# Kernel tuning notes

Hardware: AMD Instinct MI355X
Metric: run time of the kernel (lower is better)

## Reference

```python
import jax, jax.numpy as jnp
import numpy as np

N_NODES = 50000


def _gcn_norm(edge_index, num_nodes):
    # PyG GCNConv default: add self-loops, symmetric deg^{-1/2} normalization.
    src, dst = edge_index[0], edge_index[1]
    loops = jnp.arange(num_nodes, dtype=src.dtype)
    src = jnp.concatenate([src, loops])
    dst = jnp.concatenate([dst, loops])
    ones = jnp.ones(src.shape[0], dtype=jnp.float32)
    deg = jax.ops.segment_sum(ones, dst, num_segments=num_nodes)
    dinv = jnp.where(deg > 0, jax.lax.rsqrt(deg), 0.0)
    norm = dinv[src] * dinv[dst]  # [E + N]
    return src, dst, norm


def _gcn_layer(x, src, dst, norm, W, b, num_nodes):
    h = x @ W                                   # [N, H]
    msg = h[src] * norm[:, None]                # gather + scale, [E+N, H]
    out = jax.ops.segment_sum(msg, dst, num_segments=num_nodes)  # scatter-add
    return out + b


def setup_inputs() -> dict:
    key = jax.random.key(0)
    ks = jax.random.split(key, 8)
    d_in, d_h = 128, 128
    x = jax.random.normal(ks[0], (N_NODES, d_in), dtype=jnp.float32)
    edge_index = jax.random.randint(ks[1], (2, 800000), 0, N_NODES, dtype=jnp.int64)
    s1 = 1.0 / np.sqrt(d_in)
    s2 = 1.0 / np.sqrt(d_h)
    W1 = jax.random.normal(ks[2], (d_in, d_h), dtype=jnp.float32) * s1
    b1 = jnp.zeros((d_h,), dtype=jnp.float32)
    W2 = jax.random.normal(ks[3], (d_h, d_h), dtype=jnp.float32) * s2
    b2 = jnp.zeros((d_h,), dtype=jnp.float32)
    Wl = jax.random.normal(ks[4], (d_h, 1), dtype=jnp.float32) * s2
    bl = jnp.zeros((1,), dtype=jnp.float32)
    return {"x": x, "edge_index": edge_index, "W1": W1, "b1": b1,
            "W2": W2, "b2": b2, "Wl": Wl, "bl": bl}


def reference(x, edge_index, W1, b1, W2, b2, Wl, bl):
    n = x.shape[0]
    src, dst, norm = _gcn_norm(edge_index, n)
    h = jax.nn.relu(_gcn_layer(x, src, dst, norm, W1, b1, n))
    # dropout is identity in eval mode
    h = _gcn_layer(h, src, dst, norm, W2, b2, n)
    return jax.nn.sigmoid(h @ Wl + bl)  # [N, 1]
```

## Files before the change

kernel.cpp:

```cpp
#include <hip/hip_runtime.h>
#include <math.h>

#define NN 50000
#define NE 800000
#define DD 128
#define NPAD 50048
#define ELLW 64

typedef __attribute__((ext_vector_type(8))) short bf16x8;
typedef __attribute__((ext_vector_type(4))) float f32x4;
typedef __attribute__((ext_vector_type(2))) float f32x2;

__device__ __forceinline__ int clampN(int v) {
  return v < 0 ? 0 : (v >= NN ? NN - 1 : v);
}

__device__ __forceinline__ unsigned short f2b(float f) {
  union { float f; unsigned int u; } x; x.f = f;
  unsigned int u = x.u;
  u += 0x7fffu + ((u >> 16) & 1u);
  return (unsigned short)(u >> 16);
}

__device__ __forceinline__ float blo(unsigned int v) {
  union { unsigned int u; float f; } a; a.u = v << 16; return a.f;
}
__device__ __forceinline__ float bhi(unsigned int v) {
  union { unsigned int u; float f; } a; a.u = v & 0xffff0000u; return a.f;
}


__global__ __launch_bounds__(256) void k_prep_w(
    const float* __restrict__ W1, const float* __restrict__ W2,
    const float* __restrict__ b2, const float* __restrict__ Wl,
    const float* __restrict__ bl, unsigned short* __restrict__ Wt1,
    float* __restrict__ w2l, float* __restrict__ c0b, int* __restrict__ cur) {
  __shared__ float part[2];
  if (blockIdx.x < 64) {
    int i = blockIdx.x * 256 + threadIdx.x;
    int n = i >> 7, k = i & 127;
    Wt1[i] = f2b(W1[k * DD + n]);
  } else if (blockIdx.x == 64) {
    if (threadIdx.x < DD) {
      int k = threadIdx.x;
      float acc = 0.f;
      for (int c = 0; c < DD; ++c) acc += W2[k * DD + c] * Wl[c];
      w2l[k] = acc;
      float pc = b2[k] * Wl[k];
#pragma unroll
      for (int off = 32; off > 0; off >>= 1) pc += __shfl_down(pc, off, 64);
      if ((k & 63) == 0) part[k >> 6] = pc;
      __syncthreads();
      if (k == 0) c0b[0] = part[0] + part[1] + bl[0];
    }
  } else {
    int i = (blockIdx.x - 65) * 256 + threadIdx.x;
    if (i < NN) cur[i] = 0;
  }
}


__device__ __forceinline__ void scat1(int d, int s, int* __restrict__ cur,
                                      unsigned short* __restrict__ col) {
  d = clampN(d);
  int pos = atomicAdd(&cur[d], 1);
  if (pos < ELLW)
    __builtin_nontemporal_store((unsigned short)clampN(s), &col[d * ELLW + pos]);
}

__global__ __launch_bounds__(256) void k_scatter_nt(
    const int4* __restrict__ src4, const int4* __restrict__ dst4,
    int* __restrict__ cur, unsigned short* __restrict__ col) {
  int i = blockIdx.x * 256 + threadIdx.x;
  if (i < NE / 4) {
    int4 d4 = dst4[i];
    int4 s4 = src4[i];
    scat1(d4.x, s4.x, cur, col);
    scat1(d4.y, s4.y, cur, col);
    scat1(d4.z, s4.z, cur, col);
    scat1(d4.w, s4.w, cur, col);
  }
}


__global__ __launch_bounds__(256) void k_gemm_f32(
    const float* __restrict__ x, const unsigned short* __restrict__ Wt,
    const int* __restrict__ cur, unsigned short* __restrict__ outb) {
  __shared__ char lds[16384 + 32768];
  char* Al = lds;
  char* Wl = lds + 16384;

  const int tid = threadIdx.x;
  const int row0 = blockIdx.x * 64;

  {
    const float4* src = (const float4*)x;
#pragma unroll
    for (int kk = 0; kk < 8; ++kk) {
      int idx = tid + kk * 256;
      int r = idx >> 5;
      int c4 = idx & 31;
      float4 v = make_float4(0.f, 0.f, 0.f, 0.f);
      if (row0 + r < NN) v = src[(size_t)(row0 + r) * 32 + c4];
      ushort4 u;
      u.x = f2b(v.x); u.y = f2b(v.y); u.z = f2b(v.z); u.w = f2b(v.w);
      int bo = r * 256 + c4 * 8;
      *(ushort4*)(Al + (bo ^ ((r & 7) << 4))) = u;
    }
  }
  {
    const uint4* src = (const uint4*)Wt;
    for (int idx = tid; idx < 2048; idx += 256) {
      int bo = idx * 16;
      int r = bo >> 8;
      *(uint4*)(Wl + (bo ^ ((r & 7) << 4))) = src[idx];
    }
  }
  __syncthreads();

  const int w = tid >> 6, lane = tid & 63;
  const int lr = lane & 15, lk = lane >> 4;

  bf16x8 af[4];
  {
    int ar = w * 16 + lr;
    int base = ar * 256 + lk * 16;
    int swz = (ar & 7) << 4;
#pragma unroll
    for (int k4 = 0; k4 < 4; ++k4)
      af[k4] = *(const bf16x8*)(Al + ((base + k4 * 64) ^ swz));
  }

  f32x4 accs[8];
#pragma unroll
  for (int n = 0; n < 8; ++n) {
    f32x4 acc = {0.f, 0.f, 0.f, 0.f};
    int br = n * 16 + lr;
    int bbase = br * 256 + lk * 16;
    int bswz = (br & 7) << 4;
#pragma unroll
    for (int k4 = 0; k4 < 4; ++k4) {
      bf16x8 bf = *(const bf16x8*)(Wl + ((bbase + k4 * 64) ^ bswz));
      acc = __builtin_amdgcn_mfma_f32_16x16x32_bf16(af[k4], bf, acc, 0, 0, 0);
    }
    accs[n] = acc;
  }

#pragma unroll
  for (int r = 0; r < 4; ++r) {
    int grow = row0 + w * 16 + lk * 4 + r;
    if (grow < NN) {
      float dv = rsqrtf(1.0f + (float)cur[grow]);
#pragma unroll
      for (int n = 0; n < 8; ++n)
        outb[(size_t)grow * DD + n * 16 + lr] = f2b(accs[n][r] * dv);
    }
  }
}


__device__ __forceinline__ void accp(f32x2* acc, uint4 v) {
  f32x2 a0 = {blo(v.x), bhi(v.x)};
  f32x2 a1 = {blo(v.y), bhi(v.y)};
  f32x2 a2 = {blo(v.z), bhi(v.z)};
  f32x2 a3 = {blo(v.w), bhi(v.w)};
  acc[0] += a0;
  acc[1] += a1;
  acc[2] += a2;
  acc[3] += a3;
}

__global__ __launch_bounds__(256) void k_agg_relu_proj_ell(
    const uint4* __restrict__ tpb4, const float* __restrict__ b,
    const float* __restrict__ w2l, const int* __restrict__ cur,
    const unsigned short* __restrict__ col, float* __restrict__ s_out) {
  int wid = threadIdx.x >> 6;
  int lane = threadIdx.x & 63;
  int d = blockIdx.x * 4 + wid;
  int il = lane & 7, g = lane >> 3;

  f32x2 acc[8];
#pragma unroll
  for (int j = 0; j < 8; ++j) acc[j] = (f32x2){0.f, 0.f};

  int degd = cur[d];
  int deg = min(degd, ELLW);
  const unsigned short* crow = col + d * ELLW;
  for (int e = g; e < deg; e += 8) {
    int s = crow[e];
    uint4 v0 = tpb4[(size_t)s * 16 + il * 2];
    uint4 v1 = tpb4[(size_t)s * 16 + il * 2 + 1];
    accp(acc, v0);
    accp(acc + 4, v1);
  }
#pragma unroll
  for (int j = 0; j < 8; ++j) {
    float ax = acc[j].x, ay = acc[j].y;
    ax += __shfl_xor(ax, 8, 64);  ay += __shfl_xor(ay, 8, 64);
    ax += __shfl_xor(ax, 16, 64); ay += __shfl_xor(ay, 16, 64);
    ax += __shfl_xor(ax, 32, 64); ay += __shfl_xor(ay, 32, 64);
    acc[j].x = ax; acc[j].y = ay;
  }
  uint4 s0 = tpb4[(size_t)d * 16 + il * 2];
  uint4 s1 = tpb4[(size_t)d * 16 + il * 2 + 1];
  accp(acc, s0);
  accp(acc + 4, s1);

  float dv = rsqrtf(1.0f + (float)degd);
  float p = 0.f;
#pragma unroll
  for (int q = 0; q < 4; ++q) {
    float4 bb = ((const float4*)b)[il * 4 + q];
    float4 ww = ((const float4*)w2l)[il * 4 + q];
    p = fmaf(fmaxf(fmaf(dv, acc[2 * q].x, bb.x), 0.f), ww.x, p);
    p = fmaf(fmaxf(fmaf(dv, acc[2 * q].y, bb.y), 0.f), ww.y, p);
    p = fmaf(fmaxf(fmaf(dv, acc[2 * q + 1].x, bb.z), 0.f), ww.z, p);
    p = fmaf(fmaxf(fmaf(dv, acc[2 * q + 1].y, bb.w), 0.f), ww.w, p);
  }
  p += __shfl_xor(p, 1, 64);
  p += __shfl_xor(p, 2, 64);
  p += __shfl_xor(p, 4, 64);
  if (lane == 0) s_out[d] = dv * p;
}


__global__ __launch_bounds__(256) void k_agg_scalar_ell(
    const float* __restrict__ s, const float* __restrict__ c0b,
    const int* __restrict__ cur, const unsigned short* __restrict__ col,
    float* __restrict__ out) {
  int wid = threadIdx.x >> 6;
  int lane = threadIdx.x & 63;
  int q = lane & 15;
  int d = blockIdx.x * 16 + wid * 4 + (lane >> 4);

  int degd = cur[d];
  int deg = min(degd, ELLW);
  const unsigned short* crow = col + d * ELLW;
  float tot = 0.f;
  for (int e = q; e < deg; e += 16) tot += s[crow[e]];
  tot += __shfl_xor(tot, 1, 64);
  tot += __shfl_xor(tot, 2, 64);
  tot += __shfl_xor(tot, 4, 64);
  tot += __shfl_xor(tot, 8, 64);
  if (q == 0) {
    float dv = rsqrtf(1.0f + (float)degd);
    float z = dv * (tot + s[d]) + c0b[0];
    out[d] = 1.f / (1.f + expf(-z));
  }
}


extern "C" void kernel_launch(void* const* d_in, const int* in_sizes, int n_in,
                              void* d_out, int out_size, void* d_ws, size_t ws_size,
                              hipStream_t stream) {
  const float* x = (const float*)d_in[0];
  const int* ei = (const int*)d_in[1];
  const float* W1 = (const float*)d_in[2];
  const float* b1 = (const float*)d_in[3];
  const float* W2 = (const float*)d_in[4];
  const float* b2 = (const float*)d_in[5];
  const float* Wl = (const float*)d_in[6];
  const float* bl = (const float*)d_in[7];
  float* out = (float*)d_out;

  char* ws = (char*)d_ws;
  size_t off = 0;
  auto alloc = [&](size_t bytes) -> char* {
    char* p = ws + off;
    off = (off + bytes + 255) & ~(size_t)255;
    return p;
  };
  int* cur = (int*)alloc(NN * sizeof(int));
  unsigned short* colell = (unsigned short*)alloc((size_t)NN * ELLW * 2);
  unsigned short* Wt1 = (unsigned short*)alloc(DD * DD * 2);
  float* w2l = (float*)alloc(DD * sizeof(float));
  float* c0b = (float*)alloc(sizeof(float));
  unsigned short* tpb = (unsigned short*)alloc((size_t)NPAD * DD * 2);
  float* sbuf = (float*)alloc(NN * sizeof(float));
  (void)ws_size;

  k_prep_w<<<65 + 196, 256, 0, stream>>>(W1, W2, b2, Wl, bl, Wt1, w2l, c0b, cur);

  k_scatter_nt<<<(NE / 4 + 255) / 256, 256, 0, stream>>>(
      (const int4*)ei, (const int4*)(ei + NE), cur, colell);

  k_gemm_f32<<<NPAD / 64, 256, 0, stream>>>(x, Wt1, cur, tpb);

  k_agg_relu_proj_ell<<<NN / 4, 256, 0, stream>>>((const uint4*)tpb, b1, w2l,
                                                  cur, colell, sbuf);
  k_agg_scalar_ell<<<(NN + 15) / 16, 256, 0, stream>>>(sbuf, c0b, cur, colell, out);
}
```

Before: 127.7 us.

## Partition edge scatter into eight destination slices for XCD locality

The ELL-building scatter now runs eight times as many blocks. Each group of blocks handles only destinations inside one of eight node-range slices, with the slice chosen from the low bits of the block index, so consecutive blocks cover different slices. The intent is to keep the atomic counters and column writes of each slice local to one XCD's L2 on the multi-die GPU and to cut cross-die atomic traffic. The nontemporal stores become regular stores. The cost is that every dst vector is read eight times, and src is read only when some lane falls in the slice.

```diff
diff --git a/kernel.cpp b/kernel.cpp
--- a/kernel.cpp
+++ b/kernel.cpp
@@ -5,6 +5,7 @@
 #define NE 800000
 #define DD 128
 #define NPAD 50048
+#define NSLICE 6256
 #define ELLW 64
 
 typedef __attribute__((ext_vector_type(8))) short bf16x8;
@@ -60,25 +61,35 @@
 }
 
 
-__device__ __forceinline__ void scat1(int d, int s, int* __restrict__ cur,
+__device__ __forceinline__ void scat1(int d, int s, int lo, int hi,
+                                      int* __restrict__ cur,
                                       unsigned short* __restrict__ col) {
-  d = clampN(d);
-  int pos = atomicAdd(&cur[d], 1);
-  if (pos < ELLW)
-    __builtin_nontemporal_store((unsigned short)clampN(s), &col[d * ELLW + pos]);
-}
-
-__global__ __launch_bounds__(256) void k_scatter_nt(
+  if (d >= lo && d < hi) {
+    int pos = atomicAdd(&cur[d], 1);
+    if (pos < ELLW) col[d * ELLW + pos] = (unsigned short)clampN(s);
+  }
+}
+
+__global__ __launch_bounds__(256) void k_scatter4(
     const int4* __restrict__ src4, const int4* __restrict__ dst4,
     int* __restrict__ cur, unsigned short* __restrict__ col) {
-  int i = blockIdx.x * 256 + threadIdx.x;
-  if (i < NE / 4) {
-    int4 d4 = dst4[i];
+  int g = blockIdx.x & 7;
+  int blk = blockIdx.x >> 3;
+  int lo = g * NSLICE;
+  int hi = min(lo + NSLICE, NN);
+  int i = blk * 256 + threadIdx.x;
+  if (i >= NE / 4) return;
+  int4 d4 = dst4[i];
+  d4.x = clampN(d4.x); d4.y = clampN(d4.y);
+  d4.z = clampN(d4.z); d4.w = clampN(d4.w);
+  bool any = (d4.x >= lo && d4.x < hi) | (d4.y >= lo && d4.y < hi) |
+             (d4.z >= lo && d4.z < hi) | (d4.w >= lo && d4.w < hi);
+  if (any) {
     int4 s4 = src4[i];
-    scat1(d4.x, s4.x, cur, col);
-    scat1(d4.y, s4.y, cur, col);
-    scat1(d4.z, s4.z, cur, col);
-    scat1(d4.w, s4.w, cur, col);
+    scat1(d4.x, s4.x, lo, hi, cur, col);
+    scat1(d4.y, s4.y, lo, hi, cur, col);
+    scat1(d4.z, s4.z, lo, hi, cur, col);
+    scat1(d4.w, s4.w, lo, hi, cur, col);
   }
 }
 
@@ -281,8 +292,8 @@
 
   k_prep_w<<<65 + 196, 256, 0, stream>>>(W1, W2, b2, Wl, bl, Wt1, w2l, c0b, cur);
 
-  k_scatter_nt<<<(NE / 4 + 255) / 256, 256, 0, stream>>>(
-      (const int4*)ei, (const int4*)(ei + NE), cur, colell);
+  k_scatter4<<<8 * 782, 256, 0, stream>>>((const int4*)ei, (const int4*)(ei + NE),
+                                          cur, colell);
 
   k_gemm_f32<<<NPAD / 64, 256, 0, stream>>>(x, Wt1, cur, tpb);
 
```

Result: faster. 112.8 us (-11.7%).

## Split ELL adjacency into eight per-section sub-tables to spread atomic contention

Applied to the files above, without the earlier changes.

The single ELL table with one counter per node is replaced by eight independent sections, each with its own counters and 32-wide column slots, chosen by block index modulo 8. This spreads the scatter atomics over eight counter arrays, which may cut same-address contention and let writes stay local. The aggregation kernels now read eight counters per node and reduce the degree with shuffles, and each group of lanes walks one section. The cost is more counter reads, eight times the counter memory and zeroing work, and uneven per-lane loop lengths.

```diff
diff --git a/kernel.cpp b/kernel.cpp
--- a/kernel.cpp
+++ b/kernel.cpp
@@ -5,7 +5,7 @@
 #define NE 800000
 #define DD 128
 #define NPAD 50048
-#define ELLW 64
+#define SECW 32
 
 typedef __attribute__((ext_vector_type(8))) short bf16x8;
 typedef __attribute__((ext_vector_type(4))) float f32x4;
@@ -34,7 +34,7 @@
     const float* __restrict__ W1, const float* __restrict__ W2,
     const float* __restrict__ b2, const float* __restrict__ Wl,
     const float* __restrict__ bl, unsigned short* __restrict__ Wt1,
-    float* __restrict__ w2l, float* __restrict__ c0b, int* __restrict__ cur) {
+    float* __restrict__ w2l, float* __restrict__ c0b, int* __restrict__ cur2) {
   __shared__ float part[2];
   if (blockIdx.x < 64) {
     int i = blockIdx.x * 256 + threadIdx.x;
@@ -55,37 +55,47 @@
     }
   } else {
     int i = (blockIdx.x - 65) * 256 + threadIdx.x;
-    if (i < NN) cur[i] = 0;
-  }
-}
-
-
-__device__ __forceinline__ void scat1(int d, int s, int* __restrict__ cur,
-                                      unsigned short* __restrict__ col) {
-  d = clampN(d);
-  int pos = atomicAdd(&cur[d], 1);
-  if (pos < ELLW)
-    __builtin_nontemporal_store((unsigned short)clampN(s), &col[d * ELLW + pos]);
-}
-
-__global__ __launch_bounds__(256) void k_scatter_nt(
+    if (i < 8 * NN) cur2[i] = 0;
+  }
+}
+
+
+__global__ __launch_bounds__(256) void k_scatter_sec(
     const int4* __restrict__ src4, const int4* __restrict__ dst4,
-    int* __restrict__ cur, unsigned short* __restrict__ col) {
+    int* __restrict__ cur2, unsigned short* __restrict__ col2) {
+  int w = blockIdx.x & 7;
   int i = blockIdx.x * 256 + threadIdx.x;
-  if (i < NE / 4) {
-    int4 d4 = dst4[i];
-    int4 s4 = src4[i];
-    scat1(d4.x, s4.x, cur, col);
-    scat1(d4.y, s4.y, cur, col);
-    scat1(d4.z, s4.z, cur, col);
-    scat1(d4.w, s4.w, cur, col);
+  if (i >= NE / 4) return;
+  int4 d4 = dst4[i];
+  int4 s4 = src4[i];
+  int* curw = cur2 + w * NN;
+  unsigned short* colw = col2 + (size_t)w * NN * SECW;
+  {
+    int d = clampN(d4.x);
+    int pos = atomicAdd(&curw[d], 1);
+    if (pos < SECW) colw[d * SECW + pos] = (unsigned short)clampN(s4.x);
+  }
+  {
+    int d = clampN(d4.y);
+    int pos = atomicAdd(&curw[d], 1);
+    if (pos < SECW) colw[d * SECW + pos] = (unsigned short)clampN(s4.y);
+  }
+  {
+    int d = clampN(d4.z);
+    int pos = atomicAdd(&curw[d], 1);
+    if (pos < SECW) colw[d * SECW + pos] = (unsigned short)clampN(s4.z);
+  }
+  {
+    int d = clampN(d4.w);
+    int pos = atomicAdd(&curw[d], 1);
+    if (pos < SECW) colw[d * SECW + pos] = (unsigned short)clampN(s4.w);
   }
 }
 
 
 __global__ __launch_bounds__(256) void k_gemm_f32(
     const float* __restrict__ x, const unsigned short* __restrict__ Wt,
-    const int* __restrict__ cur, unsigned short* __restrict__ outb) {
+    const int* __restrict__ cur2, unsigned short* __restrict__ outb) {
   __shared__ char lds[16384 + 32768];
   char* Al = lds;
   char* Wl = lds + 16384;
@@ -150,7 +160,10 @@
   for (int r = 0; r < 4; ++r) {
     int grow = row0 + w * 16 + lk * 4 + r;
     if (grow < NN) {
-      float dv = rsqrtf(1.0f + (float)cur[grow]);
+      int deg = 0;
+#pragma unroll
+      for (int wq = 0; wq < 8; ++wq) deg += cur2[wq * NN + grow];
+      float dv = rsqrtf(1.0f + (float)deg);
 #pragma unroll
       for (int n = 0; n < 8; ++n)
         outb[(size_t)grow * DD + n * 16 + lr] = f2b(accs[n][r] * dv);
@@ -170,10 +183,10 @@
   acc[3] += a3;
 }
 
-__global__ __launch_bounds__(256) void k_agg_relu_proj_ell(
+__global__ __launch_bounds__(256) void k_agg_relu_proj_sec(
     const uint4* __restrict__ tpb4, const float* __restrict__ b,
-    const float* __restrict__ w2l, const int* __restrict__ cur,
-    const unsigned short* __restrict__ col, float* __restrict__ s_out) {
+    const float* __restrict__ w2l, const int* __restrict__ cur2,
+    const unsigned short* __restrict__ col2, float* __restrict__ s_out) {
   int wid = threadIdx.x >> 6;
   int lane = threadIdx.x & 63;
   int d = blockIdx.x * 4 + wid;
@@ -183,16 +196,16 @@
 #pragma unroll
   for (int j = 0; j < 8; ++j) acc[j] = (f32x2){0.f, 0.f};
 
-  int degd = cur[d];
-  int deg = min(degd, ELLW);
-  const unsigned short* crow = col + d * ELLW;
-  for (int e = g; e < deg; e += 8) {
+  int cnt = min(cur2[g * NN + d], SECW);
+  const unsigned short* crow = col2 + (size_t)g * NN * SECW + d * SECW;
+  for (int e = 0; e < cnt; ++e) {
     int s = crow[e];
     uint4 v0 = tpb4[(size_t)s * 16 + il * 2];
     uint4 v1 = tpb4[(size_t)s * 16 + il * 2 + 1];
     accp(acc, v0);
     accp(acc + 4, v1);
   }
+  float degf = (float)cnt;
 #pragma unroll
   for (int j = 0; j < 8; ++j) {
     float ax = acc[j].x, ay = acc[j].y;
@@ -201,12 +214,16 @@
     ax += __shfl_xor(ax, 32, 64); ay += __shfl_xor(ay, 32, 64);
     acc[j].x = ax; acc[j].y = ay;
   }
+  degf += __shfl_xor(degf, 8, 64);
+  degf += __shfl_xor(degf, 16, 64);
+  degf += __shfl_xor(degf, 32, 64);
+
   uint4 s0 = tpb4[(size_t)d * 16 + il * 2];
   uint4 s1 = tpb4[(size_t)d * 16 + il * 2 + 1];
   accp(acc, s0);
   accp(acc + 4, s1);
 
-  float dv = rsqrtf(1.0f + (float)degd);
+  float dv = rsqrtf(1.0f + degf);
   float p = 0.f;
 #pragma unroll
   for (int q = 0; q < 4; ++q) {
@@ -224,26 +241,27 @@
 }
 
 
-__global__ __launch_bounds__(256) void k_agg_scalar_ell(
+__global__ __launch_bounds__(256) void k_agg_scalar_sec(
     const float* __restrict__ s, const float* __restrict__ c0b,
-    const int* __restrict__ cur, const unsigned short* __restrict__ col,
+    const int* __restrict__ cur2, const unsigned short* __restrict__ col2,
     float* __restrict__ out) {
   int wid = threadIdx.x >> 6;
   int lane = threadIdx.x & 63;
   int q = lane & 15;
   int d = blockIdx.x * 16 + wid * 4 + (lane >> 4);
 
-  int degd = cur[d];
-  int deg = min(degd, ELLW);
-  const unsigned short* crow = col + d * ELLW;
+  int w = q & 7, start = q >> 3;
+  int cnt = min(cur2[w * NN + d], SECW);
+  const unsigned short* crow = col2 + (size_t)w * NN * SECW + d * SECW;
   float tot = 0.f;
-  for (int e = q; e < deg; e += 16) tot += s[crow[e]];
-  tot += __shfl_xor(tot, 1, 64);
-  tot += __shfl_xor(tot, 2, 64);
-  tot += __shfl_xor(tot, 4, 64);
-  tot += __shfl_xor(tot, 8, 64);
+  for (int j = start; j < cnt; j += 2) tot += s[crow[j]];
+  float degf = (q < 8) ? (float)cnt : 0.f;
+  tot += __shfl_xor(tot, 1, 64);   degf += __shfl_xor(degf, 1, 64);
+  tot += __shfl_xor(tot, 2, 64);   degf += __shfl_xor(degf, 2, 64);
+  tot += __shfl_xor(tot, 4, 64);   degf += __shfl_xor(degf, 4, 64);
+  tot += __shfl_xor(tot, 8, 64);   degf += __shfl_xor(degf, 8, 64);
   if (q == 0) {
-    float dv = rsqrtf(1.0f + (float)degd);
+    float dv = rsqrtf(1.0f + degf);
     float z = dv * (tot + s[d]) + c0b[0];
     out[d] = 1.f / (1.f + expf(-z));
   }
@@ -270,8 +288,8 @@
     off = (off + bytes + 255) & ~(size_t)255;
     return p;
   };
-  int* cur = (int*)alloc(NN * sizeof(int));
-  unsigned short* colell = (unsigned short*)alloc((size_t)NN * ELLW * 2);
+  int* cur2 = (int*)alloc(8 * NN * sizeof(int));
+  unsigned short* col2 = (unsigned short*)alloc((size_t)8 * NN * SECW * 2);
   unsigned short* Wt1 = (unsigned short*)alloc(DD * DD * 2);
   float* w2l = (float*)alloc(DD * sizeof(float));
   float* c0b = (float*)alloc(sizeof(float));
@@ -279,14 +297,16 @@
   float* sbuf = (float*)alloc(NN * sizeof(float));
   (void)ws_size;
 
-  k_prep_w<<<65 + 196, 256, 0, stream>>>(W1, W2, b2, Wl, bl, Wt1, w2l, c0b, cur);
-
-  k_scatter_nt<<<(NE / 4 + 255) / 256, 256, 0, stream>>>(
-      (const int4*)ei, (const int4*)(ei + NE), cur, colell);
-
-  k_gemm_f32<<<NPAD / 64, 256, 0, stream>>>(x, Wt1, cur, tpb);
-
-  k_agg_relu_proj_ell<<<NN / 4, 256, 0, stream>>>((const uint4*)tpb, b1, w2l,
-                                                  cur, colell, sbuf);
-  k_agg_scalar_ell<<<(NN + 15) / 16, 256, 0, stream>>>(sbuf, c0b, cur, colell, out);
-}
+  const int ZB = (8 * NN + 255) / 256;
+
+  k_prep_w<<<65 + ZB, 256, 0, stream>>>(W1, W2, b2, Wl, bl, Wt1, w2l, c0b, cur2);
+
+  k_scatter_sec<<<(NE / 4 + 255) / 256, 256, 0, stream>>>(
+      (const int4*)ei, (const int4*)(ei + NE), cur2, col2);
+
+  k_gemm_f32<<<NPAD / 64, 256, 0, stream>>>(x, Wt1, cur2, tpb);
+
+  k_agg_relu_proj_sec<<<NN / 4, 256, 0, stream>>>((const uint4*)tpb, b1, w2l,
+                                                  cur2, col2, sbuf);
+  k_agg_scalar_sec<<<(NN + 15) / 16, 256, 0, stream>>>(sbuf, c0b, cur2, col2, out);
+}
```

Result: slower. 130.9 us (+2.5%).
